# Kernel optimization log

Hardware: AMD Instinct MI355X
Metric: run time of the kernel (lower is better)

## Reference

```python
import jax, jax.numpy as jnp
import numpy as np

B, L, D, H, DH = 2, 2048, 1024, 16, 64
THETA_T = 100.0
EPS_COS = 1e-6
EPS_NORM = 1e-6


def make_rope_tables(n_heads=H, d_head=DH, theta_t=THETA_T):
    dr = d_head // 12                      # 5 rotary freqs per head per axis
    n = n_heads * dr
    log_min, log_max = np.log(np.pi), np.log(10.0 * np.pi)
    f = np.exp(np.linspace(log_min, log_max, n + 1)[:-1])
    freqs = np.stack([f, f]).reshape(2, dr, n_heads).transpose(0, 2, 1)   # (2, H, dr)
    t_freqs = (theta_t ** (-np.arange(n, dtype=np.float64) / n)).reshape(dr, n_heads).T  # (H, dr)
    return jnp.asarray(freqs, jnp.float32), jnp.asarray(t_freqs, jnp.float32)


def rms_norm(x, scale, eps=EPS_NORM):
    ms = jnp.mean(x.astype(jnp.float32) ** 2, axis=-1, keepdims=True)
    return x * (scale.astype(jnp.float32) * jax.lax.rsqrt(ms + eps)).astype(x.dtype)


def rope_theta(pos, pos_orig, time, freqs, t_freqs):
    # pos_to_use: (b, l, c=2, xy=2), mapped to [-1, 1]
    pos_use = jnp.stack([pos_orig, pos], axis=2) * 2.0 - 1.0
    theta_w = pos_use[..., 0][:, :, :, None, None] * freqs[0]      # b l 2 H dr
    theta_h = pos_use[..., 1][:, :, :, None, None] * freqs[1]      # b l 2 H dr
    theta_t = time[:, :, None, None, None] * t_freqs               # b l 1 H dr
    theta = jnp.concatenate([theta_h, theta_w, theta_t], axis=2)   # b l 5 H dr
    b, l = theta.shape[0], theta.shape[1]
    theta = jnp.transpose(theta, (0, 1, 3, 2, 4)).reshape(b, l, H, -1)  # b l H (5*dr)
    return theta


def apply_rotary_emb(x, theta):
    d = theta.shape[-1]
    x1, x2, x3 = x[..., :d], x[..., d:2 * d], x[..., 2 * d:]
    cos, sin = jnp.cos(theta), jnp.sin(theta)
    y1 = x1 * cos - x2 * sin
    y2 = x2 * cos + x1 * sin
    return jnp.concatenate([y1, y2, x3], axis=-1)


def scale_for_cosine_sim(q, k, scale, eps=EPS_COS):
    sq = jnp.sum(q * q, axis=-1, keepdims=True)
    sk = jnp.sum(k * k, axis=-1, keepdims=True)
    sqrt_scale = jnp.sqrt(scale)                         # (H,1,1) -> broadcasts to (b,H,l,1)
    return q * (sqrt_scale * jax.lax.rsqrt(sq + eps)), k * (sqrt_scale * jax.lax.rsqrt(sk + eps))


def setup_inputs() -> dict:
    key = jax.random.key(0)
    ks = jax.random.split(key, 8)
    return {
        "x": jax.random.normal(ks[0], (B, L, D), jnp.float32),
        "pos": jax.random.uniform(ks[1], (B, L, 2), jnp.float32),
        "pos_orig": jax.random.uniform(ks[2], (B, L, 2), jnp.float32),
        "time": jax.random.uniform(ks[3], (B, L), jnp.float32),
        "w_qkv": jax.random.normal(ks[4], (3 * D, D), jnp.float32) * (D ** -0.5),
        "w_out": jax.random.normal(ks[5], (D, D), jnp.float32) * (D ** -0.5),
        "w_up": jax.random.normal(ks[6], (4 * D, D), jnp.float32) * (D ** -0.5),
        "w_down": jax.random.normal(ks[7], (D, 4 * D), jnp.float32) * ((4 * D) ** -0.5),
        "norm1_scale": jnp.ones((D,), jnp.float32),
        "norm2_scale": jnp.ones((D,), jnp.float32),
        "qk_scale": jnp.full((H, 1, 1), 10.0, jnp.float32),
    }


def reference(x, pos, pos_orig, time, w_qkv, w_out, w_up, w_down,
              norm1_scale, norm2_scale, qk_scale):
    freqs, t_freqs = make_rope_tables()
    b, l, _ = x.shape

    # --- attention block (pre-norm) ---
    xn = rms_norm(x, norm1_scale)
    qkv = jnp.einsum('bld,ed->ble', xn, w_qkv)                  # b l 3D
    q, k, v = jnp.split(qkv, 3, axis=-1)
    q = q.reshape(b, l, H, DH)
    k = k.reshape(b, l, H, DH)
    v = v.reshape(b, l, H, DH).transpose(0, 2, 1, 3)            # b H l dh

    theta = rope_theta(pos, pos_orig, time, freqs, t_freqs)      # b l H 25
    q = apply_rotary_emb(q, theta).transpose(0, 2, 1, 3)         # b H l dh
    k = apply_rotary_emb(k, theta).transpose(0, 2, 1, 3)

    q, k = scale_for_cosine_sim(q, k, qk_scale)                  # cosine-sim QK norm
    scores = jnp.einsum('bhqd,bhkd->bhqk', q, k)                 # scale=1 (already folded in)
    probs = jax.nn.softmax(scores, axis=-1)
    attn = jnp.einsum('bhqk,bhkd->bhqd', probs, v)
    attn = attn.transpose(0, 2, 1, 3).reshape(b, l, D)
    x = x + jnp.einsum('bld,ed->ble', attn, w_out)

    h = rms_norm(x, norm2_scale)
    h = jax.nn.gelu(jnp.einsum('bld,ed->ble', h, w_up), approximate=True)
    x = x + jnp.einsum('ble,de->bld', h, w_down)
    return x
```

## Files before the change

### kernel.cpp

```cpp
#include <hip/hip_runtime.h>

#define B_ 2
#define L_ 2048
#define D_ 1024
#define H_ 16
#define DH_ 64

typedef float f32x4 __attribute__((ext_vector_type(4)));
typedef __bf16 bf16x8 __attribute__((ext_vector_type(8)));

__device__ __forceinline__ ushort f2bf(float f) {
  unsigned u = __float_as_uint(f);
  u += 0x7fffu + ((u >> 16) & 1u);
  return (ushort)(u >> 16);
}
__device__ __forceinline__ float bf2f(ushort h) {
  return __uint_as_float(((unsigned)h) << 16);
}

__device__ __forceinline__ void gload_lds16(const void* g, void* l) {
  __builtin_amdgcn_global_load_lds(
      (const __attribute__((address_space(1))) unsigned*)g,
      (__attribute__((address_space(3))) unsigned*)l, 16, 0, 0);
}

__global__ __launch_bounds__(256) void cast_all_kernel(const float* __restrict__ w0,
                                                       const float* __restrict__ w1,
                                                       const float* __restrict__ w2,
                                                       const float* __restrict__ w3,
                                                       ushort* __restrict__ o0,
                                                       ushort* __restrict__ o1,
                                                       ushort* __restrict__ o2,
                                                       ushort* __restrict__ o3) {
  int i = blockIdx.x * 256 + threadIdx.x;
  const float* src;
  ushort* dst;
  int j = i;
  if (j < 786432) { src = w0; dst = o0; }
  else if (j < 786432 + 262144) { j -= 786432; src = w1; dst = o1; }
  else if (j < 786432 + 262144 + 1048576) { j -= 786432 + 262144; src = w2; dst = o2; }
  else { j -= 786432 + 262144 + 1048576; src = w3; dst = o3; }
  float4 v = ((const float4*)src)[j];
  ushort4 o;
  o.x = f2bf(v.x); o.y = f2bf(v.y); o.z = f2bf(v.z); o.w = f2bf(v.w);
  ((ushort4*)dst)[j] = o;
}

template <typename T>
__global__ __launch_bounds__(256) void rmsnorm_kernel(const T* __restrict__ x,
                                                      const float* __restrict__ scale,
                                                      ushort* __restrict__ out) {
  int row = blockIdx.x, t = threadIdx.x;
  float4 v;
  if constexpr (sizeof(T) == 4) {
    v = ((const float4*)((const float*)x + (size_t)row * D_))[t];
  } else {
    ushort4 u = ((const ushort4*)((const ushort*)x + (size_t)row * D_))[t];
    v.x = bf2f(u.x); v.y = bf2f(u.y); v.z = bf2f(u.z); v.w = bf2f(u.w);
  }
  float ss = v.x * v.x + v.y * v.y + v.z * v.z + v.w * v.w;
#pragma unroll
  for (int d = 1; d < 64; d <<= 1) ss += __shfl_xor(ss, d);
  __shared__ float wsum[4];
  if ((t & 63) == 0) wsum[t >> 6] = ss;
  __syncthreads();
  float tot = wsum[0] + wsum[1] + wsum[2] + wsum[3];
  float r = rsqrtf(tot * (1.0f / D_) + 1e-6f);
  float4 sc = ((const float4*)scale)[t];
  ushort4 o;
  o.x = f2bf(v.x * sc.x * r); o.y = f2bf(v.y * sc.y * r);
  o.z = f2bf(v.z * sc.z * r); o.w = f2bf(v.w * sc.w * r);
  ((ushort4*)(out + (size_t)row * D_))[t] = o;
}

template <int EPI, int BM, int BN, int DEPTH, int XR, int XC, bool CTFAST>
__global__ __launch_bounds__(256) void gemm_nt(const ushort* __restrict__ A,
                                               const ushort* __restrict__ Bw,
                                               void* __restrict__ Cout,
                                               const void* __restrict__ resid,
                                               int M, int N, int K) {
  constexpr int WROWS = BM / 2, WCOLS = BN / 2;
  constexpr int MR = WROWS / 16, NR = WCOLS / 16;
  constexpr int ALOADS = BM / 64, BLOADS = BN / 64;
  constexpr int NLOADS = ALOADS + BLOADS;
  __shared__ __align__(16) ushort Als[DEPTH][BM * 32];
  __shared__ __align__(16) ushort Bls[DEPTH][BN * 32];
  const int tid = threadIdx.x;
  const int lane = tid & 63;
  const int w = tid >> 6;
  const int wr = w >> 1, wc = w & 1;
  const int bid = blockIdx.y * gridDim.x + blockIdx.x;
  const int xcd = bid & 7;
  const int i0 = bid >> 3;
  const int CR = gridDim.x / XR, CC = gridDim.y / XC;
  int rt, ct;
  if constexpr (CTFAST) {
    rt = (xcd % XR) * CR + (i0 / CC);
    ct = (xcd / XR) * CC + (i0 % CC);
  } else {
    rt = (xcd % XR) * CR + (i0 % CR);
    ct = (xcd / XR) * CC + (i0 / CR);
  }
  const int row0 = rt * BM;
  const int col0 = ct * BN;
  const ushort* Ab = A + (size_t)row0 * K;
  const ushort* Bb = Bw + (size_t)col0 * K;
  const int sr = tid >> 2;
  const int scA = (((tid & 3) ^ ((tid >> 3) & 3)) * 8);
  const int fr = lane & 15;
  const int fg = lane >> 4;
  f32x4 zero = {0.f, 0.f, 0.f, 0.f};
  f32x4 acc[MR][NR];
#pragma unroll
  for (int m = 0; m < MR; m++)
#pragma unroll
    for (int n = 0; n < NR; n++) acc[m][n] = zero;

  auto stage = [&](int slot, int kt) {
#pragma unroll
    for (int i2 = 0; i2 < ALOADS; i2++)
      gload_lds16(Ab + (size_t)(sr + 64 * i2) * K + kt + scA, &Als[slot][i2 * 2048 + tid * 8]);
#pragma unroll
    for (int i2 = 0; i2 < BLOADS; i2++)
      gload_lds16(Bb + (size_t)(sr + 64 * i2) * K + kt + scA, &Bls[slot][i2 * 2048 + tid * 8]);
  };
  const int nt = K >> 5;
#pragma unroll
  for (int p = 0; p < DEPTH - 1; p++) stage(p, p << 5);
  int cur = 0, sbuf = DEPTH - 1;
  for (int t = 0; t < nt; t++) {
    const int ahead = nt - 1 - t;
    if constexpr (DEPTH == 3) {
      if (ahead >= 1) asm volatile("s_waitcnt vmcnt(%0)" ::"i"(NLOADS) : "memory");
      else            asm volatile("s_waitcnt vmcnt(0)" ::: "memory");
    } else {
      if (ahead >= 3)      asm volatile("s_waitcnt vmcnt(%0)" ::"i"(3 * NLOADS) : "memory");
      else if (ahead == 2) asm volatile("s_waitcnt vmcnt(%0)" ::"i"(2 * NLOADS) : "memory");
      else if (ahead == 1) asm volatile("s_waitcnt vmcnt(%0)" ::"i"(NLOADS) : "memory");
      else                 asm volatile("s_waitcnt vmcnt(0)" ::: "memory");
    }
    __builtin_amdgcn_s_barrier();
    __builtin_amdgcn_sched_barrier(0);
    if (t + DEPTH - 1 < nt) {
      stage(sbuf, (t + DEPTH - 1) << 5);
      sbuf = (sbuf == DEPTH - 1) ? 0 : sbuf + 1;
    }
    bf16x8 af[MR], bfr[NR];
#pragma unroll
    for (int m = 0; m < MR; m++) {
      int rA = wr * WROWS + m * 16 + fr;
      af[m] = *(const bf16x8*)&Als[cur][rA * 32 + ((fg ^ ((rA >> 1) & 3)) << 3)];
    }
#pragma unroll
    for (int n = 0; n < NR; n++) {
      int rB = wc * WCOLS + n * 16 + fr;
      bfr[n] = *(const bf16x8*)&Bls[cur][rB * 32 + ((fg ^ ((rB >> 1) & 3)) << 3)];
    }
    __builtin_amdgcn_s_setprio(1);
#pragma unroll
    for (int m = 0; m < MR; m++)
#pragma unroll
      for (int n = 0; n < NR; n++)
        acc[m][n] = __builtin_amdgcn_mfma_f32_16x16x32_bf16(af[m], bfr[n], acc[m][n], 0, 0, 0);
    __builtin_amdgcn_s_setprio(0);
    cur = (cur == DEPTH - 1) ? 0 : cur + 1;
  }
  const int orow = row0 + wr * WROWS + fg * 4;
  const int ocol = col0 + wc * WCOLS + fr;
#pragma unroll
  for (int m = 0; m < MR; m++) {
#pragma unroll
    for (int j = 0; j < 4; j++) {
      int r = orow + m * 16 + j;
#pragma unroll
      for (int n = 0; n < NR; n++) {
        int cidx = ocol + n * 16;
        size_t idx = (size_t)r * N + cidx;
        float v = acc[m][n][j];
        if (EPI == 0) {
          ((ushort*)Cout)[idx] = f2bf(v);
        } else if (EPI == 1) {
          ((ushort*)Cout)[idx] = f2bf(((const float*)resid)[idx] + v);
        } else if (EPI == 2) {
          float g = 0.5f * v * (1.0f + tanhf(0.7978845608f * (v + 0.044715f * v * v * v)));
          ((ushort*)Cout)[idx] = f2bf(g);
        } else {
          ((float*)Cout)[idx] = bf2f(((const ushort*)resid)[idx]) + v;
        }
      }
    }
  }
}

__global__ __launch_bounds__(256) void rope_kernel(const ushort* __restrict__ qkv,
                                                   const float* __restrict__ pos,
                                                   const float* __restrict__ pos_orig,
                                                   const float* __restrict__ timep,
                                                   const float* __restrict__ qk_scale,
                                                   ushort* __restrict__ qr,
                                                   ushort* __restrict__ kr) {
  int gw = (blockIdx.x * 256 + threadIdx.x) >> 6;
  int lane = threadIdx.x & 63;
  int h = gw & 15;
  int row = gw >> 4;
  int b = row >> 11;
  int l = row & (L_ - 1);
  float qv = bf2f(qkv[(size_t)row * 3072 + h * 64 + lane]);
  float kv = bf2f(qkv[(size_t)row * 3072 + 1024 + h * 64 + lane]);
  float c = 1.0f, s = 0.0f;
  if (lane < 50) {
    int idx = lane < 25 ? lane : lane - 25;
    int sg = idx / 5, d = idx % 5;
    int fi = d * 16 + h;
    float th;
    if (sg == 4) {
      th = timep[row] * __expf(-(float)fi * 0.05756462732485115f);
    } else {
      float fr = 3.14159265358979323846f * __expf((float)fi * 0.028782313662425575f);
      const float* psrc = (sg == 0 || sg == 2) ? pos_orig : pos;
      int comp = (sg < 2) ? 1 : 0;
      th = (2.0f * psrc[(size_t)row * 2 + comp] - 1.0f) * fr;
    }
    s = sinf(th);
    c = cosf(th);
  }
  int partner = lane < 25 ? lane + 25 : lane - 25;
  float qp = __shfl(qv, partner, 64);
  float kp = __shfl(kv, partner, 64);
  float yq, yk;
  if (lane < 25) { yq = qv * c - qp * s; yk = kv * c - kp * s; }
  else if (lane < 50) { yq = qv * c + qp * s; yk = kv * c + kp * s; }
  else { yq = qv; yk = kv; }
  float sq = yq * yq, sk = yk * yk;
#pragma unroll
  for (int d = 1; d < 64; d <<= 1) { sq += __shfl_xor(sq, d); sk += __shfl_xor(sk, d); }
  float scl = sqrtf(qk_scale[h]);
  float qo = yq * scl * rsqrtf(sq + 1e-6f);
  float ko = yk * scl * rsqrtf(sk + 1e-6f);
  size_t o = ((size_t)(b * 16 + h) * L_ + l) * 64 + lane;
  qr[o] = f2bf(qo);
  kr[o] = f2bf(ko);
}

__global__ __launch_bounds__(256) void vtrans_kernel(const ushort* __restrict__ qkv,
                                                     ushort* __restrict__ vT) {
  __shared__ __align__(16) ushort tile[64][72];
  int t = threadIdx.x;
  int lt = blockIdx.x;
  int bh = blockIdx.y;
  int b = bh >> 4, h = bh & 15;
  int r = t >> 3, c0 = (t & 7) * 8;
#pragma unroll
  for (int half = 0; half < 2; half++) {
    const ushort* src =
        qkv + (size_t)(b * L_ + lt * 64 + r + half * 32) * 3072 + 2048 + h * 64 + c0;
    *(uint4*)&tile[r + half * 32][c0] = *(const uint4*)src;
  }
  __syncthreads();
#pragma unroll
  for (int half = 0; half < 2; half++) {
    int dh = r + half * 32;
    unsigned p0 = (unsigned)tile[c0 + 0][dh] | ((unsigned)tile[c0 + 1][dh] << 16);
    unsigned p1 = (unsigned)tile[c0 + 2][dh] | ((unsigned)tile[c0 + 3][dh] << 16);
    unsigned p2 = (unsigned)tile[c0 + 4][dh] | ((unsigned)tile[c0 + 5][dh] << 16);
    unsigned p3 = (unsigned)tile[c0 + 6][dh] | ((unsigned)tile[c0 + 7][dh] << 16);
    uint4 o; o.x = p0; o.y = p1; o.z = p2; o.w = p3;
    *(uint4*)&vT[((size_t)bh * 64 + dh) * L_ + lt * 64 + c0] = o;
  }
}

__global__ __launch_bounds__(256) void attn_kernel(const ushort* __restrict__ qr,
                                                   const ushort* __restrict__ kr,
                                                   const ushort* __restrict__ vT,
                                                   ushort* __restrict__ attnb) {
  __shared__ __align__(16) ushort Kls[2][64 * 64];
  __shared__ __align__(16) ushort Vls[2][64 * 64];
  __shared__ __align__(16) ushort Pls[4][16 * 64];
  const int tid = threadIdx.x, lane = tid & 63, w = tid >> 6;
  const int bid = blockIdx.y * gridDim.x + blockIdx.x;
  const int qt = (bid >> 3) & 31;
  const int bh = (bid & 7) | ((bid >> 8) << 3);
  const int b = bh >> 4;
  const int fr = lane & 15, fg = lane >> 4;
  const ushort* Qb = qr + ((size_t)bh * L_ + qt * 64 + w * 16) * 64;
  bf16x8 qf[2];
#pragma unroll
  for (int c = 0; c < 2; c++)
    qf[c] = *(const bf16x8*)(Qb + fr * 64 + c * 32 + fg * 8);
  f32x4 zero = {0.f, 0.f, 0.f, 0.f};
  f32x4 accO[4];
#pragma unroll
  for (int n = 0; n < 4; n++) accO[n] = zero;
  float lrow[4] = {0.f, 0.f, 0.f, 0.f};
  const int sr = tid >> 3;
  const int scz = (((tid & 7) ^ (sr & 7)) * 8);
  auto stage = [&](int buf, int kt) {
    gload_lds16(kr + ((size_t)bh * L_ + kt + sr) * 64 + scz, &Kls[buf][tid * 8]);
    gload_lds16(kr + ((size_t)bh * L_ + kt + 32 + sr) * 64 + scz, &Kls[buf][2048 + tid * 8]);
    gload_lds16(vT + ((size_t)bh * 64 + sr) * L_ + kt + scz, &Vls[buf][tid * 8]);
    gload_lds16(vT + ((size_t)bh * 64 + 32 + sr) * L_ + kt + scz, &Vls[buf][2048 + tid * 8]);
  };
  stage(0, 0);
  int cur = 0;
  for (int t = 0; t < (L_ >> 6); t++) {
    asm volatile("s_waitcnt vmcnt(0)" ::: "memory");
    __builtin_amdgcn_s_barrier();
    __builtin_amdgcn_sched_barrier(0);
    if (t + 1 < (L_ >> 6)) stage(cur ^ 1, (t + 1) << 6);
    f32x4 sv[4];
#pragma unroll
    for (int n = 0; n < 4; n++) sv[n] = zero;
    __builtin_amdgcn_s_setprio(1);
#pragma unroll
    for (int c = 0; c < 2; c++) {
#pragma unroll
      for (int n = 0; n < 4; n++) {
        bf16x8 kf =
            *(const bf16x8*)&Kls[cur][(n * 16 + fr) * 64 + (((c * 4 + fg) ^ (fr & 7)) << 3)];
        sv[n] = __builtin_amdgcn_mfma_f32_16x16x32_bf16(qf[c], kf, sv[n], 0, 0, 0);
      }
    }
    __builtin_amdgcn_s_setprio(0);
#pragma unroll
    for (int n = 0; n < 4; n++)
#pragma unroll
      for (int j = 0; j < 4; j++) {
        float p = __expf(sv[n][j] - 12.0f);
        sv[n][j] = p;
        lrow[j] += p;
      }
#pragma unroll
    for (int j = 0; j < 4; j++) {
      int row = fg * 4 + j;
      int rbase = row * 64;
      int rx = row & 7;
#pragma unroll
      for (int n = 0; n < 4; n++) {
        int chunk = 2 * n + (fr >> 3);
        Pls[w][rbase + ((chunk ^ rx) << 3) + (fr & 7)] =
            (ushort)(__float_as_uint(sv[n][j]) >> 16);
      }
    }
    __builtin_amdgcn_s_setprio(1);
#pragma unroll
    for (int c = 0; c < 2; c++) {
      bf16x8 pa = *(const bf16x8*)&Pls[w][fr * 64 + (((c * 4 + fg) ^ (fr & 7)) << 3)];
#pragma unroll
      for (int n = 0; n < 4; n++) {
        bf16x8 vb =
            *(const bf16x8*)&Vls[cur][(n * 16 + fr) * 64 + (((c * 4 + fg) ^ (fr & 7)) << 3)];
        accO[n] = __builtin_amdgcn_mfma_f32_16x16x32_bf16(pa, vb, accO[n], 0, 0, 0);
      }
    }
    __builtin_amdgcn_s_setprio(0);
    cur ^= 1;
  }
#pragma unroll
  for (int j = 0; j < 4; j++) {
#pragma unroll
    for (int d = 1; d < 16; d <<= 1) lrow[j] += __shfl_xor(lrow[j], d);
    lrow[j] = 1.0f / lrow[j];
  }
#pragma unroll
  for (int n = 0; n < 4; n++) {
#pragma unroll
    for (int j = 0; j < 4; j++) {
      float o = accO[n][j] * lrow[j];
      int qrow = qt * 64 + w * 16 + fg * 4 + j;
      int dh = fr + n * 16;
      attnb[(size_t)(b * L_ + qrow) * 1024 + (bh & 15) * 64 + dh] = f2bf(o);
    }
  }
}

extern "C" void kernel_launch(void* const* d_in, const int* in_sizes, int n_in,
                              void* d_out, int out_size, void* d_ws, size_t ws_size,
                              hipStream_t stream) {
  const float* x = (const float*)d_in[0];
  const float* pos = (const float*)d_in[1];
  const float* pos_orig = (const float*)d_in[2];
  const float* timep = (const float*)d_in[3];
  const float* w_qkv = (const float*)d_in[4];
  const float* w_out = (const float*)d_in[5];
  const float* w_up = (const float*)d_in[6];
  const float* w_down = (const float*)d_in[7];
  const float* norm1 = (const float*)d_in[8];
  const float* norm2 = (const float*)d_in[9];
  const float* qk_scale = (const float*)d_in[10];
  float* out = (float*)d_out;
  char* ws = (char*)d_ws;
  size_t off = 0;
  auto alloc = [&](size_t bytes) {
    void* p = ws + off;
    off += bytes;
    return p;
  };
  ushort* xn = (ushort*)alloc(8ull << 20);
  ushort* qkvb = (ushort*)alloc(32ull << 20);
  ushort* qrb = (ushort*)alloc(8ull << 20);
  ushort* krb = (ushort*)alloc(8ull << 20);
  ushort* vTb = (ushort*)alloc(8ull << 20);
  ushort* attnb = (ushort*)alloc(8ull << 20);
  ushort* x1b = (ushort*)alloc(8ull << 20);
  ushort* wqkvb = (ushort*)alloc(6ull << 20);
  ushort* woutb = (ushort*)alloc(2ull << 20);
  ushort* wupb = (ushort*)alloc(8ull << 20);
  ushort* wdownb = (ushort*)alloc(8ull << 20);

  cast_all_kernel<<<12288, 256, 0, stream>>>(w_qkv, w_out, w_up, w_down,
                                             wqkvb, woutb, wupb, wdownb);

  rmsnorm_kernel<float><<<4096, 256, 0, stream>>>(x, norm1, xn);
  gemm_nt<0, 128, 128, 3, 4, 2, false><<<dim3(32, 24), 256, 0, stream>>>(
      xn, wqkvb, qkvb, nullptr, 4096, 3072, 1024);
  rope_kernel<<<16384, 256, 0, stream>>>(qkvb, pos, pos_orig, timep, qk_scale, qrb, krb);
  vtrans_kernel<<<dim3(32, 32), 256, 0, stream>>>(qkvb, vTb);
  attn_kernel<<<dim3(32, 32), 256, 0, stream>>>(qrb, krb, vTb, attnb);
  gemm_nt<1, 64, 64, 5, 4, 2, false><<<dim3(64, 16), 256, 0, stream>>>(
      attnb, woutb, x1b, x, 4096, 1024, 1024);
  rmsnorm_kernel<ushort><<<4096, 256, 0, stream>>>(x1b, norm2, xn);
  gemm_nt<2, 128, 128, 3, 4, 2, false><<<dim3(32, 32), 256, 0, stream>>>(
      xn, wupb, qkvb, nullptr, 4096, 4096, 1024);
  gemm_nt<3, 64, 64, 5, 4, 2, true><<<dim3(64, 16), 256, 0, stream>>>(
      qkvb, wdownb, out, x1b, 4096, 1024, 4096);
}
```

Before: 293.2 us.

## Split-K the down-projection GEMM with larger tiles and a separate reduction kernel

The down-projection GEMM (K=4096) changes from 64x64 tiles to 128x128 tiles and splits K into two halves across blockIdx.z. Each half writes fp32 partials into reused workspace, and a new reduction kernel sums the two partials with the bf16 residual. The larger tiles raise data reuse, and split-K keeps 512 blocks in the grid. The cost is an extra 32 MB of fp32 partial writes and reads plus one more kernel launch.

```diff
diff --git a/kernel.cpp b/kernel.cpp
--- a/kernel.cpp
+++ b/kernel.cpp
@@ -78,7 +78,7 @@
                                                const ushort* __restrict__ Bw,
                                                void* __restrict__ Cout,
                                                const void* __restrict__ resid,
-                                               int M, int N, int K) {
+                                               int M, int N, int K, int Klen) {
   constexpr int WROWS = BM / 2, WCOLS = BN / 2;
   constexpr int MR = WROWS / 16, NR = WCOLS / 16;
   constexpr int ALOADS = BM / 64, BLOADS = BN / 64;
@@ -103,8 +103,9 @@
   }
   const int row0 = rt * BM;
   const int col0 = ct * BN;
-  const ushort* Ab = A + (size_t)row0 * K;
-  const ushort* Bb = Bw + (size_t)col0 * K;
+  const int koff = blockIdx.z * Klen;
+  const ushort* Ab = A + (size_t)row0 * K + koff;
+  const ushort* Bb = Bw + (size_t)col0 * K + koff;
   const int sr = tid >> 2;
   const int scA = (((tid & 3) ^ ((tid >> 3) & 3)) * 8);
   const int fr = lane & 15;
@@ -124,7 +125,7 @@
     for (int i2 = 0; i2 < BLOADS; i2++)
       gload_lds16(Bb + (size_t)(sr + 64 * i2) * K + kt + scA, &Bls[slot][i2 * 2048 + tid * 8]);
   };
-  const int nt = K >> 5;
+  const int nt = Klen >> 5;
 #pragma unroll
   for (int p = 0; p < DEPTH - 1; p++) stage(p, p << 5);
   int cur = 0, sbuf = DEPTH - 1;
@@ -167,6 +168,7 @@
   }
   const int orow = row0 + wr * WROWS + fg * 4;
   const int ocol = col0 + wc * WCOLS + fr;
+  float* Pz = (float*)Cout + (size_t)blockIdx.z * M * N;
 #pragma unroll
   for (int m = 0; m < MR; m++) {
 #pragma unroll
@@ -184,12 +186,30 @@
         } else if (EPI == 2) {
           float g = 0.5f * v * (1.0f + tanhf(0.7978845608f * (v + 0.044715f * v * v * v)));
           ((ushort*)Cout)[idx] = f2bf(g);
+        } else if (EPI == 3) {
+          ((float*)Cout)[idx] = bf2f(((const ushort*)resid)[idx]) + v;
         } else {
-          ((float*)Cout)[idx] = bf2f(((const ushort*)resid)[idx]) + v;
+          Pz[idx] = v;
         }
       }
     }
   }
+}
+
+__global__ __launch_bounds__(256) void reduce_down_kernel(const float* __restrict__ P0,
+                                                          const float* __restrict__ P1,
+                                                          const ushort* __restrict__ residb,
+                                                          float* __restrict__ out) {
+  int i = blockIdx.x * 256 + threadIdx.x;
+  float4 a = ((const float4*)P0)[i];
+  float4 b = ((const float4*)P1)[i];
+  ushort4 r = ((const ushort4*)residb)[i];
+  float4 o;
+  o.x = a.x + b.x + bf2f(r.x);
+  o.y = a.y + b.y + bf2f(r.y);
+  o.z = a.z + b.z + bf2f(r.z);
+  o.w = a.w + b.w + bf2f(r.w);
+  ((float4*)out)[i] = o;
 }
 
 __global__ __launch_bounds__(256) void rope_kernel(const ushort* __restrict__ qkv,
@@ -406,21 +426,23 @@
   ushort* woutb = (ushort*)alloc(2ull << 20);
   ushort* wupb = (ushort*)alloc(8ull << 20);
   ushort* wdownb = (ushort*)alloc(8ull << 20);
+  float* Ppart = (float*)qrb;
 
   cast_all_kernel<<<12288, 256, 0, stream>>>(w_qkv, w_out, w_up, w_down,
                                              wqkvb, woutb, wupb, wdownb);
 
   rmsnorm_kernel<float><<<4096, 256, 0, stream>>>(x, norm1, xn);
   gemm_nt<0, 128, 128, 3, 4, 2, false><<<dim3(32, 24), 256, 0, stream>>>(
-      xn, wqkvb, qkvb, nullptr, 4096, 3072, 1024);
+      xn, wqkvb, qkvb, nullptr, 4096, 3072, 1024, 1024);
   rope_kernel<<<16384, 256, 0, stream>>>(qkvb, pos, pos_orig, timep, qk_scale, qrb, krb);
   vtrans_kernel<<<dim3(32, 32), 256, 0, stream>>>(qkvb, vTb);
   attn_kernel<<<dim3(32, 32), 256, 0, stream>>>(qrb, krb, vTb, attnb);
   gemm_nt<1, 64, 64, 5, 4, 2, false><<<dim3(64, 16), 256, 0, stream>>>(
-      attnb, woutb, x1b, x, 4096, 1024, 1024);
+      attnb, woutb, x1b, x, 4096, 1024, 1024, 1024);
   rmsnorm_kernel<ushort><<<4096, 256, 0, stream>>>(x1b, norm2, xn);
   gemm_nt<2, 128, 128, 3, 4, 2, false><<<dim3(32, 32), 256, 0, stream>>>(
-      xn, wupb, qkvb, nullptr, 4096, 4096, 1024);
-  gemm_nt<3, 64, 64, 5, 4, 2, true><<<dim3(64, 16), 256, 0, stream>>>(
-      qkvb, wdownb, out, x1b, 4096, 1024, 4096);
-}
+      xn, wupb, qkvb, nullptr, 4096, 4096, 1024, 1024);
+  gemm_nt<4, 128, 128, 3, 4, 2, true><<<dim3(32, 8, 2), 256, 0, stream>>>(
+      qkvb, wdownb, Ppart, nullptr, 4096, 1024, 4096, 2048);
+  reduce_down_kernel<<<4096, 256, 0, stream>>>(Ppart, Ppart + (4u << 20), x1b, out);
+}
```

New measurement: 285.2 us. 1.03x faster.
